# Kernel optimization log

Measured on AMD Instinct MI355X. Metric: run time of the kernel, lower is better.

Reference implementation:

```python
import jax, jax.numpy as jnp
import numpy as np


def setup_inputs() -> dict:
    key = jax.random.key(0)
    k1, k2 = jax.random.split(key)
    B, V, D, C, F = 4, 50000, 16, 16, 16
    inputs = jax.random.normal(k1, (B, V, D, C), dtype=jnp.float32)
    # kernel shape (ndirs, nchannels, nfilters) as in build(); glorot-ish scale
    kernel = jax.random.normal(k2, (D, C, F), dtype=jnp.float32) * (1.0 / np.sqrt(D * C))
    bias = jnp.zeros((F,), dtype=jnp.float32)
    return {"inputs": inputs, "kernel": kernel, "bias": bias}


def reference(inputs, kernel, bias):
    # inputs: [B, V, D, C]; kernel: [D, C, F]; bias: [F]
    B, V, D, C = inputs.shape
    y = inputs.reshape(B * V, D, C)
    # circular extension along the direction axis: length 2*D-1
    y = jnp.concatenate([y, y[:, :-1, :]], axis=1)
    # valid conv1d with full-width kernel -> D outputs per vertex (circular correlation)
    y = jax.lax.conv_general_dilated(
        y, kernel, window_strides=(1,), padding="VALID",
        dimension_numbers=("NWC", "WIO", "NWC"))  # [B*V, D, F]
    y = y.reshape(B, V, D, -1) + bias  # bias add
    y = jax.nn.relu(y)
    # take_max=True: max-pool over the directions axis
    return jnp.max(y, axis=2)  # [B, V, F]
```

## Files before the change

### kernel.cpp

```cpp
#include <hip/hip_runtime.h>


typedef __attribute__((ext_vector_type(8))) short  bf16x8;
typedef __attribute__((ext_vector_type(4))) float  f32x4;

struct us4 { unsigned short a, b, c, d; };

__device__ __forceinline__ unsigned short f32_to_bf16(float f) {
    unsigned int u = __builtin_bit_cast(unsigned int, f);
    u += 0x7FFFu + ((u >> 16) & 1u);
    return (unsigned short)(u >> 16);
}

__global__ __launch_bounds__(256) void build_wt(
    const float* __restrict__ kern,
    unsigned short* __restrict__ wh)
{
    int n = blockIdx.x;
    int k = threadIdx.x;
    int f = n >> 4, i = n & 15;
    int d = k >> 4, c = k & 15;
    int w = (d - i) & 15;
    wh[(n << 8) + k] = f32_to_bf16(kern[(w << 8) + (c << 4) + f]);
}

__global__ __launch_bounds__(512) void ffconv_mfma(
    const float* __restrict__ x,
    const unsigned short* __restrict__ wh_g,
    const float* __restrict__ bias,
    float* __restrict__ out,
    int M)
{
    __shared__ unsigned short XH[128 * 64];
    __shared__ unsigned short WH[256 * 64];
    __shared__ float OUTS[128 * 16];

    const int tid  = threadIdx.x;
    const int lane = tid & 63;
    const int wid  = tid >> 6;
    const int wm   = wid >> 1;
    const int wn   = wid & 1;
    const int l15  = lane & 15;
    const int l4   = lane >> 4;
    const int v0   = blockIdx.x * 128;

    f32x4 acc[2][8];
    #pragma unroll
    for (int rm = 0; rm < 2; ++rm)
        #pragma unroll
        for (int cn = 0; cn < 8; ++cn)
            acc[rm][cn] = (f32x4){0.f, 0.f, 0.f, 0.f};

    for (int kc = 0; kc < 4; ++kc) {
        if (kc > 0) __syncthreads();

        #pragma unroll
        for (int q = 0; q < 4; ++q) {
            int e  = (q * 512 + tid) * 4;
            int r  = e >> 6;
            int kk = e & 63;
            float4 xv = {0.f, 0.f, 0.f, 0.f};
            if (v0 + r < M)
                xv = *reinterpret_cast<const float4*>(
                    x + (size_t)(v0 + r) * 256 + kc * 64 + kk);
            us4 h;
            h.a = f32_to_bf16(xv.x);
            h.b = f32_to_bf16(xv.y);
            h.c = f32_to_bf16(xv.z);
            h.d = f32_to_bf16(xv.w);
            int si = r * 64 + (kk ^ ((r & 7) << 3));
            *reinterpret_cast<us4*>(XH + si) = h;
        }

        #pragma unroll
        for (int q = 0; q < 8; ++q) {
            int e  = (q * 512 + tid) * 4;
            int n  = e >> 6;
            int kk = e & 63;
            us4 vh = *reinterpret_cast<const us4*>(
                wh_g + (size_t)n * 256 + kc * 64 + kk);
            int sj = n * 64 + (kk ^ ((n & 7) << 3));
            *reinterpret_cast<us4*>(WH + sj) = vh;
        }

        __syncthreads();

        #pragma unroll
        for (int ks = 0; ks < 2; ++ks) {
            int kb = ks * 32 + l4 * 8;
            bf16x8 ah[2];
            #pragma unroll
            for (int rm = 0; rm < 2; ++rm) {
                int r  = wm * 32 + rm * 16 + l15;
                int si = r * 64 + (kb ^ ((r & 7) << 3));
                ah[rm] = *reinterpret_cast<const bf16x8*>(XH + si);
            }
            #pragma unroll
            for (int cn = 0; cn < 8; ++cn) {
                int n  = wn * 128 + cn * 16 + l15;
                int sj = n * 64 + (kb ^ ((n & 7) << 3));
                bf16x8 bh = *reinterpret_cast<const bf16x8*>(WH + sj);
                #pragma unroll
                for (int rm = 0; rm < 2; ++rm)
                    acc[rm][cn] = __builtin_amdgcn_mfma_f32_16x16x32_bf16(
                        ah[rm], bh, acc[rm][cn], 0, 0, 0);
            }
        }
    }

    #pragma unroll
    for (int rm = 0; rm < 2; ++rm) {
        #pragma unroll
        for (int cn = 0; cn < 8; ++cn) {
            float mx[4];
            #pragma unroll
            for (int q = 0; q < 4; ++q) {
                float v = acc[rm][cn][q];
                v = fmaxf(v, __shfl_xor(v, 1));
                v = fmaxf(v, __shfl_xor(v, 2));
                v = fmaxf(v, __shfl_xor(v, 4));
                v = fmaxf(v, __shfl_xor(v, 8));
                mx[q] = v;
            }
            if (l15 == 0) {
                int f = wn * 8 + cn;
                float bf = bias[f];
                #pragma unroll
                for (int q = 0; q < 4; ++q) {
                    int r = wm * 32 + rm * 16 + l4 * 4 + q;
                    OUTS[r * 16 + f] = fmaxf(mx[q] + bf, 0.f);
                }
            }
        }
    }
    __syncthreads();

    {
        int e  = tid * 4;
        int r  = e >> 4;
        int f0 = e & 15;
        if (v0 + r < M)
            *reinterpret_cast<float4*>(out + (size_t)(v0 + r) * 16 + f0) =
                *reinterpret_cast<const float4*>(OUTS + e);
    }
}

extern "C" void kernel_launch(void* const* d_in, const int* in_sizes, int n_in,
                              void* d_out, int out_size, void* d_ws, size_t ws_size,
                              hipStream_t stream) {
    const float* x    = (const float*)d_in[0];
    const float* kern = (const float*)d_in[1];
    const float* bias = (const float*)d_in[2];
    float* out        = (float*)d_out;

    unsigned short* wh = (unsigned short*)d_ws;

    const int M = in_sizes[0] / 256;

    hipLaunchKernelGGL(build_wt, dim3(256), dim3(256), 0, stream, kern, wh);

    const int blocks = (M + 127) / 128;
    hipLaunchKernelGGL(ffconv_mfma, dim3(blocks), dim3(512), 0, stream,
                       x, wh, bias, out, M);
}
```

Before: 372.6 us.

## Load X directly into registers with double-buffered prefetch, stage full weights in LDS once

The kernel no longer stages X through shared memory. Each lane loads its MFMA A-operand rows straight from global memory into registers and converts them to bf16 there. Those loads are double-buffered across the four K chunks, so the next chunk's global loads overlap the current chunk's MFMAs. The whole 256x256 bf16 weight matrix (128KB of LDS) is loaded once, which leaves a single barrier instead of one per chunk. The cost is heavy LDS use, which limits occupancy to about one block per CU, plus more register pressure from the two float4[8] buffers and less coalesced global X reads.

```diff
diff --git a/kernel.cpp b/kernel.cpp
--- a/kernel.cpp
+++ b/kernel.cpp
@@ -1,15 +1,23 @@
 #include <hip/hip_runtime.h>
 
 
-typedef __attribute__((ext_vector_type(8))) short  bf16x8;
-typedef __attribute__((ext_vector_type(4))) float  f32x4;
-
-struct us4 { unsigned short a, b, c, d; };
+typedef __attribute__((ext_vector_type(8))) short          bf16x8;
+typedef __attribute__((ext_vector_type(4))) float          f32x4;
+typedef __attribute__((ext_vector_type(8))) unsigned short us8;
 
 __device__ __forceinline__ unsigned short f32_to_bf16(float f) {
     unsigned int u = __builtin_bit_cast(unsigned int, f);
     u += 0x7FFFu + ((u >> 16) & 1u);
     return (unsigned short)(u >> 16);
+}
+
+__device__ __forceinline__ bf16x8 cvt8(float4 a, float4 b) {
+    bf16x8 r;
+    r[0] = (short)f32_to_bf16(a.x); r[1] = (short)f32_to_bf16(a.y);
+    r[2] = (short)f32_to_bf16(a.z); r[3] = (short)f32_to_bf16(a.w);
+    r[4] = (short)f32_to_bf16(b.x); r[5] = (short)f32_to_bf16(b.y);
+    r[6] = (short)f32_to_bf16(b.z); r[7] = (short)f32_to_bf16(b.w);
+    return r;
 }
 
 __global__ __launch_bounds__(256) void build_wt(
@@ -24,6 +32,36 @@
     wh[(n << 8) + k] = f32_to_bf16(kern[(w << 8) + (c << 4) + f]);
 }
 
+
+#define LOADX(buf, kc) {                                                      \
+    _Pragma("unroll")                                                         \
+    for (int h = 0; h < 2; ++h) {                                             \
+        buf[0+h] = *(const float4*)(xrow0 + (kc)*64 +  0 + l4*8 + h*4);       \
+        buf[2+h] = *(const float4*)(xrow0 + (kc)*64 + 32 + l4*8 + h*4);       \
+        buf[4+h] = *(const float4*)(xrow1 + (kc)*64 +  0 + l4*8 + h*4);       \
+        buf[6+h] = *(const float4*)(xrow1 + (kc)*64 + 32 + l4*8 + h*4);       \
+    } }
+
+#define COMPUTE(buf, kc) {                                                    \
+    bf16x8 ah00 = cvt8(buf[0], buf[1]);                          \
+    bf16x8 ah01 = cvt8(buf[2], buf[3]);                          \
+    bf16x8 ah10 = cvt8(buf[4], buf[5]);                          \
+    bf16x8 ah11 = cvt8(buf[6], buf[7]);                          \
+    _Pragma("unroll")                                                         \
+    for (int ks = 0; ks < 2; ++ks) {                                          \
+        _Pragma("unroll")                                                     \
+        for (int cn = 0; cn < 8; ++cn) {                                      \
+            int n   = wn*128 + cn*16 + l15;                                   \
+            int k   = (kc)*64 + ks*32 + l4*8;                                 \
+            int idx = n*256 + (k ^ ((n & 7) << 3));                           \
+            bf16x8 bh = *(const bf16x8*)(WH + idx);                           \
+            acc[0][cn] = __builtin_amdgcn_mfma_f32_16x16x32_bf16(             \
+                ks ? ah01 : ah00, bh, acc[0][cn], 0, 0, 0);                   \
+            acc[1][cn] = __builtin_amdgcn_mfma_f32_16x16x32_bf16(             \
+                ks ? ah11 : ah10, bh, acc[1][cn], 0, 0, 0);                   \
+        }                                                                     \
+    } }
+
 __global__ __launch_bounds__(512) void ffconv_mfma(
     const float* __restrict__ x,
     const unsigned short* __restrict__ wh_g,
@@ -31,8 +69,7 @@
     float* __restrict__ out,
     int M)
 {
-    __shared__ unsigned short XH[128 * 64];
-    __shared__ unsigned short WH[256 * 64];
+    __shared__ unsigned short WH[256 * 256];
     __shared__ float OUTS[128 * 16];
 
     const int tid  = threadIdx.x;
@@ -44,6 +81,11 @@
     const int l4   = lane >> 4;
     const int v0   = blockIdx.x * 128;
 
+    int r0 = v0 + wm * 32 + l15;
+    int r1 = r0 + 16;
+    const float* xrow0 = x + (size_t)(r0 < M ? r0 : M - 1) * 256;
+    const float* xrow1 = x + (size_t)(r1 < M ? r1 : M - 1) * 256;
+
     f32x4 acc[2][8];
     #pragma unroll
     for (int rm = 0; rm < 2; ++rm)
@@ -51,62 +93,27 @@
         for (int cn = 0; cn < 8; ++cn)
             acc[rm][cn] = (f32x4){0.f, 0.f, 0.f, 0.f};
 
-    for (int kc = 0; kc < 4; ++kc) {
-        if (kc > 0) __syncthreads();
+    float4 xa[8], xb[8];
+    LOADX(xa, 0);
 
-        #pragma unroll
-        for (int q = 0; q < 4; ++q) {
-            int e  = (q * 512 + tid) * 4;
-            int r  = e >> 6;
-            int kk = e & 63;
-            float4 xv = {0.f, 0.f, 0.f, 0.f};
-            if (v0 + r < M)
-                xv = *reinterpret_cast<const float4*>(
-                    x + (size_t)(v0 + r) * 256 + kc * 64 + kk);
-            us4 h;
-            h.a = f32_to_bf16(xv.x);
-            h.b = f32_to_bf16(xv.y);
-            h.c = f32_to_bf16(xv.z);
-            h.d = f32_to_bf16(xv.w);
-            int si = r * 64 + (kk ^ ((r & 7) << 3));
-            *reinterpret_cast<us4*>(XH + si) = h;
-        }
+    #pragma unroll
+    for (int p = 0; p < 16; ++p) {
+        int e  = (p * 512 + tid) * 8;
+        int n  = e >> 8;
+        int k0 = e & 255;
+        us8 v  = *(const us8*)(wh_g + n * 256 + k0);
+        int idx = n * 256 + (k0 ^ ((n & 7) << 3));
+        *(us8*)(WH + idx) = v;
+    }
+    __syncthreads();
 
-        #pragma unroll
-        for (int q = 0; q < 8; ++q) {
-            int e  = (q * 512 + tid) * 4;
-            int n  = e >> 6;
-            int kk = e & 63;
-            us4 vh = *reinterpret_cast<const us4*>(
-                wh_g + (size_t)n * 256 + kc * 64 + kk);
-            int sj = n * 64 + (kk ^ ((n & 7) << 3));
-            *reinterpret_cast<us4*>(WH + sj) = vh;
-        }
-
-        __syncthreads();
-
-        #pragma unroll
-        for (int ks = 0; ks < 2; ++ks) {
-            int kb = ks * 32 + l4 * 8;
-            bf16x8 ah[2];
-            #pragma unroll
-            for (int rm = 0; rm < 2; ++rm) {
-                int r  = wm * 32 + rm * 16 + l15;
-                int si = r * 64 + (kb ^ ((r & 7) << 3));
-                ah[rm] = *reinterpret_cast<const bf16x8*>(XH + si);
-            }
-            #pragma unroll
-            for (int cn = 0; cn < 8; ++cn) {
-                int n  = wn * 128 + cn * 16 + l15;
-                int sj = n * 64 + (kb ^ ((n & 7) << 3));
-                bf16x8 bh = *reinterpret_cast<const bf16x8*>(WH + sj);
-                #pragma unroll
-                for (int rm = 0; rm < 2; ++rm)
-                    acc[rm][cn] = __builtin_amdgcn_mfma_f32_16x16x32_bf16(
-                        ah[rm], bh, acc[rm][cn], 0, 0, 0);
-            }
-        }
-    }
+    LOADX(xb, 1);
+    COMPUTE(xa, 0);
+    LOADX(xa, 2);
+    COMPUTE(xb, 1);
+    LOADX(xb, 3);
+    COMPUTE(xa, 2);
+    COMPUTE(xb, 3);
 
     #pragma unroll
     for (int rm = 0; rm < 2; ++rm) {
```

New measurement: 352.5 us. 1.06x faster.
